# Kernel tuning notes

Hardware: AMD Instinct MI355X
Metric: run time of the kernel (lower is better)

The kernel has to match this reference:

```python
import jax, jax.numpy as jnp
import numpy as np

B, S, T = 64, 128, 64
V, E, H, L = 32000, 512, 512, 2
PAD, BOS = 0, 1


def setup_inputs() -> dict:
    key = jax.random.key(0)
    ks = jax.random.split(key, 14)
    w = lambda k, shape: (jax.random.normal(k, shape, jnp.float32) * 0.05)
    src_emb = w(ks[0], (V, E)).at[PAD].set(0.0)
    tgt_emb = w(ks[1], (V, E)).at[PAD].set(0.0)
    enc_Wih = w(ks[2], (L, 4 * H, E))
    enc_Whh = w(ks[3], (L, 4 * H, H))
    enc_b = w(ks[4], (L, 4 * H))          # b_ih + b_hh fused
    dec_Wih = w(ks[5], (L, 4 * H, E))
    dec_Whh = w(ks[6], (L, 4 * H, H))
    dec_b = w(ks[7], (L, 4 * H))
    gen_W = w(ks[8], (V, H))
    gen_b = jnp.zeros((V,), jnp.float32)
    x_seqs = jax.random.randint(ks[9], (B, S), 0, V, jnp.int32)
    x_len = jnp.sort(jax.random.randint(ks[10], (B,), 1, S + 1, jnp.int32))[::-1]
    y_seqs = jax.random.randint(ks[11], (B, T), 0, V, jnp.int32)
    teacher = jax.random.randint(ks[12], (T - 1,), 0, 2, jnp.int32)
    return dict(x_seqs=x_seqs, x_len=x_len, y_seqs=y_seqs, teacher=teacher,
                src_emb=src_emb, tgt_emb=tgt_emb,
                enc_Wih=enc_Wih, enc_Whh=enc_Whh, enc_b=enc_b,
                dec_Wih=dec_Wih, dec_Whh=dec_Whh, dec_b=dec_b,
                gen_W=gen_W, gen_b=gen_b)


def lstm_cell(x, h, c, Wih, Whh, b):
    # torch gate order: i, f, g, o
    g = x @ Wih.T + h @ Whh.T + b
    i, f, gg, o = jnp.split(g, 4, axis=-1)
    c2 = jax.nn.sigmoid(f) * c + jax.nn.sigmoid(i) * jnp.tanh(gg)
    h2 = jax.nn.sigmoid(o) * jnp.tanh(c2)
    return h2, c2


def encode(x_seqs, x_len, src_emb, Wih, Whh, b):
    emb = src_emb[x_seqs]                                  # [B,S,E]
    mask = jnp.arange(S)[None, :] < x_len[:, None]         # [B,S] valid steps
    inp = emb.transpose(1, 0, 2)                           # [S,B,E]
    m_t = mask.T                                           # [S,B]
    hs, cs = [], []
    for l in range(L):
        def step(carry, xs, l=l):
            h, c = carry
            xt, m = xs
            h2, c2 = lstm_cell(xt, h, c, Wih[l], Whh[l], b[l])
            m = m[:, None]
            h2 = jnp.where(m, h2, h)   # freeze state past sequence length
            c2 = jnp.where(m, c2, c)
            return (h2, c2), h2
        z = jnp.zeros((B, H), inp.dtype)
        (hT, cT), out = jax.lax.scan(step, (z, z), (inp, m_t))
        inp = out
        hs.append(hT)
        cs.append(cT)
    return jnp.stack(hs), jnp.stack(cs)                    # each [L,B,H]


def reference(x_seqs, x_len, y_seqs, teacher, src_emb, tgt_emb,
              enc_Wih, enc_Whh, enc_b, dec_Wih, dec_Whh, dec_b, gen_W, gen_b):
    h0, c0 = encode(x_seqs, x_len, src_emb, enc_Wih, enc_Whh, enc_b)

    def step(carry, xs):
        h, c, inp = carry                                  # [L,B,H],[L,B,H],[B]
        y_t, tf = xs                                       # [B], scalar flag
        x = tgt_emb[inp]                                   # [B,E]
        new_h, new_c = [], []
        for l in range(L):
            hl, cl = lstm_cell(x, h[l], c[l], dec_Wih[l], dec_Whh[l], dec_b[l])
            new_h.append(hl); new_c.append(cl)
            x = hl
        logp = jax.nn.log_softmax(x @ gen_W.T + gen_b, axis=-1)   # [B,V]
        expct = jnp.take_along_axis(logp, y_t[:, None], axis=1)[:, 0]
        pred = jnp.argmax(logp, axis=1).astype(inp.dtype)
        nxt = jnp.where(tf > 0, y_t, pred)                 # scheduled sampling
        return (jnp.stack(new_h), jnp.stack(new_c), nxt), expct

    inp0 = jnp.full((B,), BOS, jnp.int32)
    _, outp = jax.lax.scan(step, (h0, c0, inp0), (y_seqs[:, 1:].T, teacher))
    return outp.T                                          # [B, T-1]
```

## Files before the change

kernel.cpp:

```cpp
#include <hip/hip_runtime.h>
#include <hip/hip_bf16.h>
#include <cstdint>
#include <cstddef>

namespace {

constexpr int B = 64, S = 128, T = 64, V = 32000, E = 512, H = 512;
constexpr int G4 = 2048;
constexpr int TM1 = T - 1;
constexpr int CHUNK = 32;
constexpr int BH = B * H;
constexpr int NT = 128;
constexpr int NTILES = V / NT;
constexpr float MARGIN = 0.02f;

typedef __attribute__((ext_vector_type(8))) short short8v;
typedef __attribute__((ext_vector_type(4))) float f32x4;

struct Partial { float top1, top2; int i1, i2; float sumexp, gold; };

__device__ __forceinline__ float sigf(float x) { return 1.0f / (1.0f + expf(-x)); }

__device__ __forceinline__ void split3(float w, __hip_bfloat16& a, __hip_bfloat16& b,
                                       __hip_bfloat16& c2) {
    a = __float2bfloat16(w);
    float r = w - __bfloat162float(a);
    b = __float2bfloat16(r);
    c2 = __float2bfloat16(r - __bfloat162float(b));
}

__global__ __launch_bounds__(256)
void split_dec_k(const float* __restrict__ Wih, const float* __restrict__ Whh,
                 const float* __restrict__ bsrc,
                 __hip_bfloat16* __restrict__ P0, __hip_bfloat16* __restrict__ P1,
                 __hip_bfloat16* __restrict__ P2, float* __restrict__ bint)
{
    int row = blockIdx.x;
    int l = row >> 11, jp = row & 2047;
    int kh = jp >> 2, g = jp & 3, src = g * 512 + kh;
    const float* wih = Wih + ((size_t)l * 2048 + src) * 512;
    const float* whh = Whh + ((size_t)l * 2048 + src) * 512;
    size_t ro = (size_t)row * 1024;
    for (int k = threadIdx.x; k < 1024; k += 256) {
        float w = (k < 512) ? whh[k] : wih[k - 512];
        __hip_bfloat16 a, b, c2; split3(w, a, b, c2);
        P0[ro + k] = a; P1[ro + k] = b; P2[ro + k] = c2;
    }
    if (threadIdx.x == 0) bint[row] = bsrc[l * 2048 + src];
}

__global__ __launch_bounds__(256)
void split_enc_k(const float* __restrict__ Whh,
                 __hip_bfloat16* __restrict__ P0, __hip_bfloat16* __restrict__ P1,
                 __hip_bfloat16* __restrict__ P2)
{
    int row = blockIdx.x;
    int l = row >> 11, jp = row & 2047;
    int kh = jp >> 2, g = jp & 3, src = g * 512 + kh;
    const float* whh = Whh + ((size_t)l * 2048 + src) * 512;
    size_t ro = (size_t)row * 512;
    for (int k = threadIdx.x; k < 512; k += 256) {
        __hip_bfloat16 a, b, c2; split3(whh[k], a, b, c2);
        P0[ro + k] = a; P1[ro + k] = b; P2[ro + k] = c2;
    }
}

__global__ __launch_bounds__(256)
void gemm_k(const float* __restrict__ A, const float* __restrict__ Wt,
            const float* __restrict__ bias, float* __restrict__ C,
            int N, int tokmode, const int* __restrict__ xseq, int m0)
{
    constexpr int K = 512, BM = 64, BN = 128, BK = 16;
    __shared__ __align__(16) float As[BK][BM + 4];
    __shared__ __align__(16) float Bs[BK][BN + 4];
    int tid = threadIdx.x;
    int bm = blockIdx.y * BM, bn = blockIdx.x * BN;
    int tx = tid & 15, ty = tid >> 4;
    float acc[4][8] = {};

    int lm = tid >> 2, lk = (tid & 3) << 2;
    const float* Arow;
    {
        int m = bm + lm;
        if (tokmode) { int mg = m0 + m; int tt = mg >> 6, b = mg & 63;
                       Arow = A + (size_t)xseq[b * S + tt] * K; }
        else Arow = A + (size_t)m * K;
    }
    int ln = tid >> 1, lkb = (tid & 1) << 3;
    const float* Brow = Wt + (size_t)(bn + ln) * K;

    for (int k0 = 0; k0 < K; k0 += BK) {
        float4 av = *(const float4*)(Arow + k0 + lk);
        As[lk + 0][lm] = av.x; As[lk + 1][lm] = av.y;
        As[lk + 2][lm] = av.z; As[lk + 3][lm] = av.w;
        float4 bv0 = *(const float4*)(Brow + k0 + lkb);
        float4 bv1 = *(const float4*)(Brow + k0 + lkb + 4);
        Bs[lkb + 0][ln] = bv0.x; Bs[lkb + 1][ln] = bv0.y;
        Bs[lkb + 2][ln] = bv0.z; Bs[lkb + 3][ln] = bv0.w;
        Bs[lkb + 4][ln] = bv1.x; Bs[lkb + 5][ln] = bv1.y;
        Bs[lkb + 6][ln] = bv1.z; Bs[lkb + 7][ln] = bv1.w;
        __syncthreads();
#pragma unroll
        for (int kk = 0; kk < BK; ++kk) {
            const float4 a4  = *(const float4*)&As[kk][ty * 4];
            const float4 b4a = *(const float4*)&Bs[kk][tx * 8];
            const float4 b4b = *(const float4*)&Bs[kk][tx * 8 + 4];
            const float a[4]  = {a4.x, a4.y, a4.z, a4.w};
            const float bb[8] = {b4a.x, b4a.y, b4a.z, b4a.w,
                                 b4b.x, b4b.y, b4b.z, b4b.w};
#pragma unroll
            for (int i = 0; i < 4; ++i)
#pragma unroll
                for (int j = 0; j < 8; ++j)
                    acc[i][j] = fmaf(a[i], bb[j], acc[i][j]);
        }
        __syncthreads();
    }
#pragma unroll
    for (int i = 0; i < 4; ++i) {
        size_t crow = (size_t)(bm + ty * 4 + i) * N;
#pragma unroll
        for (int j = 0; j < 8; ++j) {
            int cg = bn + tx * 8 + j;
            int jp = ((cg & 511) << 2) | (cg >> 9);
            C[crow + jp] = acc[i][j] + bias[cg];
        }
    }
}

template<int KHALF, bool ENC>
__global__ __launch_bounds__(256)
void step_k(const __hip_bfloat16* __restrict__ hA0, const __hip_bfloat16* __restrict__ hA1,
            const __hip_bfloat16* __restrict__ hA2,
            const __hip_bfloat16* __restrict__ xA0, const __hip_bfloat16* __restrict__ xA1,
            const __hip_bfloat16* __restrict__ xA2,
            const __hip_bfloat16* __restrict__ W0, const __hip_bfloat16* __restrict__ W1,
            const __hip_bfloat16* __restrict__ W2,
            const float* __restrict__ XcOrBias,
            const float* __restrict__ h_in, float* __restrict__ h_out,
            float* __restrict__ c,
            __hip_bfloat16* __restrict__ o0, __hip_bfloat16* __restrict__ o1,
            __hip_bfloat16* __restrict__ o2,
            float* __restrict__ out0, const int* __restrict__ x_len, int t, int tloc)
{
    __shared__ float gs[64][17];
    int tid = threadIdx.x;
    int wave = tid >> 6, lane = tid & 63;
    int lr = lane & 15, kg = (lane >> 4) * 8;
    int arow = wave * 16 + lr;
    int brow = blockIdx.x * 16 + lr;
    const int KW = 512 * KHALF;

    f32x4 acc0 = {0,0,0,0}, acc1 = {0,0,0,0}, acc2 = {0,0,0,0};
    const size_t aoff = (size_t)arow * 512 + kg;
    const size_t boff = (size_t)brow * KW + kg;

#pragma unroll
    for (int kk = 0; kk < KHALF * 16; ++kk) {
        int k0 = kk * 32;
        const __hip_bfloat16 *A0, *A1, *A2; int ka;
        if (KHALF == 2 && kk >= 16) { A0 = xA0; A1 = xA1; A2 = xA2; ka = k0 - 512; }
        else                        { A0 = hA0; A1 = hA1; A2 = hA2; ka = k0; }
        short8v a0 = *(const short8v*)(A0 + aoff + ka);
        short8v a1 = *(const short8v*)(A1 + aoff + ka);
        short8v a2 = *(const short8v*)(A2 + aoff + ka);
        short8v b0 = *(const short8v*)(W0 + boff + k0);
        short8v b1 = *(const short8v*)(W1 + boff + k0);
        short8v b2 = *(const short8v*)(W2 + boff + k0);
        acc0 = __builtin_amdgcn_mfma_f32_16x16x32_bf16(a0, b0, acc0, 0, 0, 0);
        acc1 = __builtin_amdgcn_mfma_f32_16x16x32_bf16(a0, b1, acc1, 0, 0, 0);
        acc2 = __builtin_amdgcn_mfma_f32_16x16x32_bf16(a1, b0, acc2, 0, 0, 0);
        acc0 = __builtin_amdgcn_mfma_f32_16x16x32_bf16(a1, b1, acc0, 0, 0, 0);
        acc1 = __builtin_amdgcn_mfma_f32_16x16x32_bf16(a0, b2, acc1, 0, 0, 0);
        acc2 = __builtin_amdgcn_mfma_f32_16x16x32_bf16(a2, b0, acc2, 0, 0, 0);
    }
    int rb = (lane >> 4) * 4;
#pragma unroll
    for (int r = 0; r < 4; ++r)
        gs[wave * 16 + rb + r][lr] = acc0[r] + acc1[r] + acc2[r];
    __syncthreads();

    int b = tid >> 2, khl = tid & 3;
    int khg = blockIdx.x * 4 + khl;
    float4 add;
    if (ENC) add = *(const float4*)(XcOrBias + (size_t)b * G4 + (size_t)khg * 4);
    else     add = *(const float4*)(XcOrBias + (size_t)khg * 4);
    float gi = gs[b][khl * 4 + 0] + add.x;
    float gf = gs[b][khl * 4 + 1] + add.y;
    float gg = gs[b][khl * 4 + 2] + add.z;
    float go = gs[b][khl * 4 + 3] + add.w;
    size_t idx = (size_t)b * H + khg;
    float cold = c[idx];
    float c2 = sigf(gf) * cold + sigf(gi) * tanhf(gg);
    float h2 = sigf(go) * tanhf(c2);
    if (ENC) {
        bool mk = t < x_len[b];
        if (!mk) { h2 = h_in[idx]; c2 = cold; }
    }
    h_out[idx] = h2;
    c[idx] = c2;
    __hip_bfloat16 s0, s1, s2; split3(h2, s0, s1, s2);
    o0[idx] = s0; o1[idx] = s1; o2[idx] = s2;
    if (ENC && out0) out0[(size_t)(t * B + b) * H + khg] = h2;
}

__global__ __launch_bounds__(256)
void convert_bf16_k(const float* __restrict__ src, __hip_bfloat16* __restrict__ dst, int n)
{
    int i = (blockIdx.x * 256 + threadIdx.x) * 8;
    if (i + 8 > n) return;
    float4 a = *(const float4*)(src + i);
    float4 b = *(const float4*)(src + i + 4);
    __hip_bfloat16 tmp[8];
    tmp[0] = __float2bfloat16(a.x); tmp[1] = __float2bfloat16(a.y);
    tmp[2] = __float2bfloat16(a.z); tmp[3] = __float2bfloat16(a.w);
    tmp[4] = __float2bfloat16(b.x); tmp[5] = __float2bfloat16(b.y);
    tmp[6] = __float2bfloat16(b.z); tmp[7] = __float2bfloat16(b.w);
    *(short8v*)(dst + i) = *(const short8v*)tmp;
}

__global__ __launch_bounds__(256)
void gen_fused_k(const __hip_bfloat16* __restrict__ hbf,
                 const __hip_bfloat16* __restrict__ Wbf,
                 const float* __restrict__ genb,
                 const int* __restrict__ y_seqs, int t,
                 Partial* __restrict__ part)
{
    __shared__ float lds[64][NT + 4];
    __shared__ float pv1[64][4], pv2[64][4], psum[64][4], mrow[64];
    __shared__ int   pi1[64][4], pi2[64][4];

    int tid = threadIdx.x;
    int wave = tid >> 6, lane = tid & 63;
    int n0 = blockIdx.x * NT;
    int lr = lane & 15;
    int kg = (lane >> 4) * 8;

    f32x4 acc[4][2];
    const f32x4 zero = {0.f, 0.f, 0.f, 0.f};
#pragma unroll
    for (int i = 0; i < 4; ++i)
#pragma unroll
        for (int j = 0; j < 2; ++j) acc[i][j] = zero;

    const __hip_bfloat16* Arow = hbf + (size_t)lr * 512 + kg;
    const __hip_bfloat16* Brow = Wbf + (size_t)(n0 + wave * 32 + lr) * 512 + kg;
    for (int k0 = 0; k0 < 512; k0 += 32) {
        short8v a[4], b[2];
#pragma unroll
        for (int mf = 0; mf < 4; ++mf)
            a[mf] = *(const short8v*)(Arow + (size_t)mf * 16 * 512 + k0);
#pragma unroll
        for (int nf = 0; nf < 2; ++nf)
            b[nf] = *(const short8v*)(Brow + (size_t)nf * 16 * 512 + k0);
#pragma unroll
        for (int mf = 0; mf < 4; ++mf)
#pragma unroll
            for (int nf = 0; nf < 2; ++nf)
                acc[mf][nf] = __builtin_amdgcn_mfma_f32_16x16x32_bf16(
                    a[mf], b[nf], acc[mf][nf], 0, 0, 0);
    }
#pragma unroll
    for (int nf = 0; nf < 2; ++nf) {
        int colLocal = wave * 32 + nf * 16 + lr;
        float bias = genb[n0 + colLocal];
#pragma unroll
        for (int mf = 0; mf < 4; ++mf) {
#pragma unroll
            for (int r = 0; r < 4; ++r) {
                int row = mf * 16 + (lane >> 4) * 4 + r;
                lds[row][colLocal] = acc[mf][nf][r] + bias;
            }
        }
    }
    __syncthreads();

    int row = tid >> 2, q = tid & 3;
    int cbase = q * 32;
    float v1 = -3.4e38f, v2 = -3.4e38f; int i1 = 0x7fffffff, i2 = 0x7fffffff;
    for (int c = 0; c < 32; ++c) {
        float v = lds[row][cbase + c];
        int ci = cbase + c;
        if (v > v1 || (v == v1 && ci < i1)) { v2 = v1; i2 = i1; v1 = v; i1 = ci; }
        else if (v > v2 || (v == v2 && ci < i2)) { v2 = v; i2 = ci; }
    }
    pv1[row][q] = v1; pi1[row][q] = i1; pv2[row][q] = v2; pi2[row][q] = i2;
    __syncthreads();

    float t1 = -3.4e38f, t2 = -3.4e38f; int j1 = 0x7fffffff, j2 = 0x7fffffff;
    if (q == 0) {
        for (int k = 0; k < 4; ++k) {
            float a1 = pv1[row][k]; int a1i = pi1[row][k];
            float a2 = pv2[row][k]; int a2i = pi2[row][k];
            if (a1 > t1 || (a1 == t1 && a1i < j1)) { t2 = t1; j2 = j1; t1 = a1; j1 = a1i; }
            else if (a1 > t2 || (a1 == t2 && a1i < j2)) { t2 = a1; j2 = a1i; }
            if (a2 > t1 || (a2 == t1 && a2i < j1)) { t2 = t1; j2 = j1; t1 = a2; j1 = a2i; }
            else if (a2 > t2 || (a2 == t2 && a2i < j2)) { t2 = a2; j2 = a2i; }
        }
        mrow[row] = t1;
    }
    __syncthreads();
    float m = mrow[row];
    float s = 0.f;
    for (int c = 0; c < 32; ++c) s += expf(lds[row][cbase + c] - m);
    psum[row][q] = s;
    __syncthreads();
    if (q == 0) {
        float sum = psum[row][0] + psum[row][1] + psum[row][2] + psum[row][3];
        Partial p;
        p.top1 = t1; p.top2 = t2; p.i1 = n0 + j1; p.i2 = n0 + j2;
        p.sumexp = sum; p.gold = 0.f;
        part[(size_t)blockIdx.x * B + row] = p;
    }
}

__global__ __launch_bounds__(256)
void dec_reduce2_k(const Partial* __restrict__ part,
                   const float* __restrict__ h,
                   const float* __restrict__ genW, const float* __restrict__ genb,
                   const float* __restrict__ tgt_emb,
                   const int* __restrict__ y_seqs, const int* __restrict__ teacher,
                   float* __restrict__ outp,
                   __hip_bfloat16* __restrict__ xp0, __hip_bfloat16* __restrict__ xp1,
                   __hip_bfloat16* __restrict__ xp2, int t)
{
    __shared__ float sM[256], sS[256], red[256];
    __shared__ float cV[16], rV[16];
    __shared__ int   cI[16];
    __shared__ int   cN, nxt;
    int b = blockIdx.x, tid = threadIdx.x;
    int y = y_seqs[b * T + t + 1];
    const float* hrow = h + (size_t)b * 512;

    float M = -3.4e38f;
    for (int i = tid; i < NTILES; i += 256) M = fmaxf(M, part[(size_t)i * B + b].top1);
    sM[tid] = M; __syncthreads();
    for (int o = 128; o; o >>= 1) { if (tid < o) sM[tid] = fmaxf(sM[tid], sM[tid + o]); __syncthreads(); }
    M = sM[0];
    if (tid == 0) cN = 0;
    __syncthreads();

    float Ssum = 0.f;
    for (int i = tid; i < NTILES; i += 256) {
        Partial p = part[(size_t)i * B + b];
        Ssum += p.sumexp * expf(p.top1 - M);
        if (p.top1 >= M - MARGIN) { int j = atomicAdd(&cN, 1); if (j < 16) { cV[j] = p.top1; cI[j] = p.i1; } }
        if (p.top2 >= M - MARGIN) { int j = atomicAdd(&cN, 1); if (j < 16) { cV[j] = p.top2; cI[j] = p.i2; } }
    }
    sS[tid] = Ssum; __syncthreads();
    for (int o = 128; o; o >>= 1) { if (tid < o) sS[tid] += sS[tid + o]; __syncthreads(); }
    float lse = M + logf(sS[0]);
    int nc = cN < 16 ? cN : 16;

    {
        const float* wrow = genW + (size_t)y * 512;
        float s = 0.f;
        for (int k = tid; k < 512; k += 256) s = fmaf(hrow[k], wrow[k], s);
        red[tid] = s; __syncthreads();
        for (int o = 128; o; o >>= 1) { if (tid < o) red[tid] += red[tid + o]; __syncthreads(); }
        if (tid == 0) outp[b * TM1 + t] = red[0] + genb[y] - lse;
        __syncthreads();
    }
    if (nc > 1) {
        for (int j = 0; j < nc; ++j) {
            const float* wrow = genW + (size_t)cI[j] * 512;
            float s = 0.f;
            for (int k = tid; k < 512; k += 256) s = fmaf(hrow[k], wrow[k], s);
            red[tid] = s; __syncthreads();
            for (int o = 128; o; o >>= 1) { if (tid < o) red[tid] += red[tid + o]; __syncthreads(); }
            if (tid == 0) rV[j] = red[0] + genb[cI[j]];
            __syncthreads();
        }
    }
    if (tid == 0) {
        int winner;
        if (nc == 1) winner = cI[0];
        else {
            float bv = -3.4e38f; int bi = 0x7fffffff;
            for (int j = 0; j < nc; ++j)
                if (rV[j] > bv || (rV[j] == bv && cI[j] < bi)) { bv = rV[j]; bi = cI[j]; }
            winner = bi;
        }
        nxt = (teacher[t] > 0) ? y : winner;
    }
    __syncthreads();
    int tok = nxt;
    for (int k = tid; k < 512; k += 256) {
        float w = tgt_emb[(size_t)tok * 512 + k];
        __hip_bfloat16 s0, s1, s2; split3(w, s0, s1, s2);
        xp0[(size_t)b * 512 + k] = s0;
        xp1[(size_t)b * 512 + k] = s1;
        xp2[(size_t)b * 512 + k] = s2;
    }
}

__global__ __launch_bounds__(256)
void init_x_k(const float* __restrict__ tgt_emb,
              __hip_bfloat16* __restrict__ xp0, __hip_bfloat16* __restrict__ xp1,
              __hip_bfloat16* __restrict__ xp2)
{
    int b = blockIdx.x;
    for (int k = threadIdx.x; k < 512; k += 256) {
        float w = tgt_emb[512 + k];
        __hip_bfloat16 s0, s1, s2; split3(w, s0, s1, s2);
        xp0[(size_t)b * 512 + k] = s0;
        xp1[(size_t)b * 512 + k] = s1;
        xp2[(size_t)b * 512 + k] = s2;
    }
}

}

extern "C" void kernel_launch(void* const* d_in, const int* in_sizes, int n_in,
                              void* d_out, int out_size, void* d_ws, size_t ws_size,
                              hipStream_t stream)
{
    (void)in_sizes; (void)n_in; (void)out_size;
    const int*   x_seqs  = (const int*)  d_in[0];
    const int*   x_len   = (const int*)  d_in[1];
    const int*   y_seqs  = (const int*)  d_in[2];
    const int*   teacher = (const int*)  d_in[3];
    const float* src_emb = (const float*)d_in[4];
    const float* tgt_emb = (const float*)d_in[5];
    const float* eWih    = (const float*)d_in[6];
    const float* eWhh    = (const float*)d_in[7];
    const float* eb      = (const float*)d_in[8];
    const float* dWih    = (const float*)d_in[9];
    const float* dWhh    = (const float*)d_in[10];
    const float* db      = (const float*)d_in[11];
    const float* genW    = (const float*)d_in[12];
    const float* genb    = (const float*)d_in[13];
    float* out = (float*)d_out;

    float* w = (float*)d_ws;
    size_t off = 0;
    auto take = [&](size_t n) { float* p = w + off; off += n; return p; };
    auto takeb = [&](size_t n) { return (__hip_bfloat16*)take((n + 1) / 2); };

    float* Xc     = take((size_t)CHUNK * B * G4);
    float* out0   = take((size_t)S * B * H);
    __hip_bfloat16* eP0 = takeb((size_t)2 * G4 * 512);
    __hip_bfloat16* eP1 = takeb((size_t)2 * G4 * 512);
    __hip_bfloat16* eP2 = takeb((size_t)2 * G4 * 512);
    __hip_bfloat16* dP0 = takeb((size_t)2 * G4 * 1024);
    __hip_bfloat16* dP1 = takeb((size_t)2 * G4 * 1024);
    __hip_bfloat16* dP2 = takeb((size_t)2 * G4 * 1024);
    float* bint   = take(2 * (size_t)G4);
    float* hping  = take(2 * (size_t)BH);
    float* cenc   = take(2 * (size_t)BH);
    float* decc   = take(2 * (size_t)BH);
    float* dech0  = take((size_t)BH);
    float* dech1  = take((size_t)BH);
    __hip_bfloat16* encP   = takeb((size_t)2 * 3 * BH);
    __hip_bfloat16* decL0P = takeb((size_t)2 * 3 * BH);
    __hip_bfloat16* decL1P = takeb((size_t)2 * 3 * BH);
    __hip_bfloat16* xP     = takeb((size_t)3 * BH);
    float* part_f = take((size_t)NTILES * B * 6);
    if (ws_size < off * sizeof(float)) return;

    __hip_bfloat16* Wbf = (__hip_bfloat16*)Xc;
    Partial* part = (Partial*)part_f;
    auto encPl = [&](int slot, int pl) { return encP   + ((size_t)slot * 3 + pl) * BH; };
    auto d0Pl  = [&](int slot, int pl) { return decL0P + ((size_t)slot * 3 + pl) * BH; };
    auto d1Pl  = [&](int slot, int pl) { return decL1P + ((size_t)slot * 3 + pl) * BH; };

    dim3 tpb256(256);

    split_enc_k<<<dim3(2 * G4), tpb256, 0, stream>>>(eWhh, eP0, eP1, eP2);
    split_dec_k<<<dim3(2 * G4), tpb256, 0, stream>>>(dWih, dWhh, db, dP0, dP1, dP2, bint);
    hipMemsetAsync(hping, 0, 2 * BH * sizeof(float), stream);
    hipMemsetAsync(cenc,  0, 2 * BH * sizeof(float), stream);

    for (int l = 0; l < 2; ++l) {
        const float* WihL = eWih + (size_t)l * G4 * E;
        const float* bL   = eb + l * G4;
        const __hip_bfloat16* W0 = eP0 + (size_t)l * G4 * 512;
        const __hip_bfloat16* W1 = eP1 + (size_t)l * G4 * 512;
        const __hip_bfloat16* W2 = eP2 + (size_t)l * G4 * 512;
        float* cL = cenc + (size_t)l * BH;
        float* o0 = (l == 0) ? out0 : nullptr;
        hipMemsetAsync(encP, 0, 3 * BH * sizeof(__hip_bfloat16), stream);
        for (int c0 = 0; c0 < S; c0 += CHUNK) {
            if (l == 0)
                gemm_k<<<dim3(G4 / 128, CHUNK * B / 64), tpb256, 0, stream>>>(
                    src_emb, WihL, bL, Xc, G4, 1, x_seqs, c0 * B);
            else
                gemm_k<<<dim3(G4 / 128, CHUNK * B / 64), tpb256, 0, stream>>>(
                    out0 + (size_t)c0 * B * H, WihL, bL, Xc, G4, 0, nullptr, 0);
            for (int t = c0; t < c0 + CHUNK; ++t) {
                int si = t & 1, so = (t + 1) & 1;
                step_k<1, true><<<dim3(128), tpb256, 0, stream>>>(
                    encPl(si, 0), encPl(si, 1), encPl(si, 2),
                    nullptr, nullptr, nullptr, W0, W1, W2,
                    Xc + (size_t)(t - c0) * B * G4,
                    hping + (size_t)si * BH, hping + (size_t)so * BH, cL,
                    encPl(so, 0), encPl(so, 1), encPl(so, 2),
                    o0, x_len, t, t - c0);
            }
        }
        hipMemcpyAsync((l == 0 ? decL0P : decL1P), encP,
                       3 * BH * sizeof(__hip_bfloat16), hipMemcpyDeviceToDevice, stream);
        hipMemcpyAsync(decc + (size_t)l * BH, cL, BH * sizeof(float),
                       hipMemcpyDeviceToDevice, stream);
        if (l == 0) hipMemsetAsync(hping, 0, 2 * BH * sizeof(float), stream);
    }

    convert_bf16_k<<<dim3(V * E / 2048), tpb256, 0, stream>>>(genW, Wbf, V * E);
    init_x_k<<<dim3(B), tpb256, 0, stream>>>(tgt_emb, xP, xP + BH, xP + 2 * BH);

    for (int t = 0; t < TM1; ++t) {
        int si = t & 1, so = (t + 1) & 1;
        step_k<2, false><<<dim3(128), tpb256, 0, stream>>>(
            d0Pl(si, 0), d0Pl(si, 1), d0Pl(si, 2),
            xP, xP + BH, xP + 2 * BH,
            dP0, dP1, dP2, bint,
            nullptr, dech0, decc,
            d0Pl(so, 0), d0Pl(so, 1), d0Pl(so, 2),
            nullptr, nullptr, 0, 0);
        step_k<2, false><<<dim3(128), tpb256, 0, stream>>>(
            d1Pl(si, 0), d1Pl(si, 1), d1Pl(si, 2),
            d0Pl(so, 0), d0Pl(so, 1), d0Pl(so, 2),
            dP0 + (size_t)G4 * 1024, dP1 + (size_t)G4 * 1024, dP2 + (size_t)G4 * 1024,
            bint + G4,
            nullptr, dech1, decc + BH,
            d1Pl(so, 0), d1Pl(so, 1), d1Pl(so, 2),
            nullptr, nullptr, 0, 0);
        gen_fused_k<<<dim3(NTILES), tpb256, 0, stream>>>(
            d1Pl(so, 0), Wbf, genb, y_seqs, t, part);
        dec_reduce2_k<<<dim3(B), tpb256, 0, stream>>>(
            part, dech1, genW, genb, tgt_emb, y_seqs, teacher, out,
            xP, xP + BH, xP + 2 * BH, t);
    }
}
```

Before: 10.46 ms.

## Fuse all encoder/decoder steps into one persistent kernel with grid barriers

Replaces the hundreds of per-timestep kernel launches (encoder GEMMs and steps, decoder steps, generator tiles, reductions) with one persistent kernel of 256 blocks. Stages are separated by a software grid barrier built on agent-scope atomics, and shared memory is drawn from a pool of per-stage structs. The goal is to remove launch overhead and inter-kernel gaps on the long sequential recurrence. In exchange, idle blocks wait at every barrier. The kernel also depends on all 256 blocks being co-resident, or it can deadlock. The generator stage now runs 250 tiles on 256 blocks.

```diff
diff --git a/kernel.cpp b/kernel.cpp
--- a/kernel.cpp
+++ b/kernel.cpp
@@ -13,11 +13,20 @@
 constexpr int NT = 128;
 constexpr int NTILES = V / NT;
 constexpr float MARGIN = 0.02f;
+constexpr unsigned NBLK = 256;
 
 typedef __attribute__((ext_vector_type(8))) short short8v;
 typedef __attribute__((ext_vector_type(4))) float f32x4;
 
 struct Partial { float top1, top2; int i1, i2; float sumexp, gold; };
+
+struct GemmSh { float As[16][68]; float Bs[16][132]; };
+struct StepSh { float gs[64][17]; };
+struct GenSh  { float lds[64][NT + 4]; float pv1[64][4], pv2[64][4], psum[64][4], mrow[64];
+                int pi1[64][4], pi2[64][4]; };
+struct RedSh  { float sM[256], sS[256], red[256]; float cV[16], rV[16]; int cI[16]; int cN, nxt; };
+static_assert(sizeof(GenSh) < 40960 && sizeof(GemmSh) < 40960 &&
+              sizeof(StepSh) < 40960 && sizeof(RedSh) < 40960, "shared pool");
 
 __device__ __forceinline__ float sigf(float x) { return 1.0f / (1.0f + expf(-x)); }
 
@@ -27,6 +36,24 @@
     float r = w - __bfloat162float(a);
     b = __float2bfloat16(r);
     c2 = __float2bfloat16(r - __bfloat162float(b));
+}
+
+__device__ __forceinline__ void gbar(unsigned* cnt, unsigned* gen, unsigned& ep)
+{
+    unsigned tgt = ep + 1; ep = tgt;
+    __syncthreads();
+    if (threadIdx.x == 0) {
+        unsigned prev = __hip_atomic_fetch_add(cnt, 1u, __ATOMIC_ACQ_REL, __HIP_MEMORY_SCOPE_AGENT);
+        if (prev == NBLK - 1u) {
+            __hip_atomic_store(cnt, 0u, __ATOMIC_RELAXED, __HIP_MEMORY_SCOPE_AGENT);
+            __hip_atomic_store(gen, tgt, __ATOMIC_RELEASE, __HIP_MEMORY_SCOPE_AGENT);
+        } else {
+            while (__hip_atomic_load(gen, __ATOMIC_RELAXED, __HIP_MEMORY_SCOPE_AGENT) < tgt)
+                __builtin_amdgcn_s_sleep(2);
+            __builtin_amdgcn_fence(__ATOMIC_ACQUIRE, "agent");
+        }
+    }
+    __syncthreads();
 }
 
 __global__ __launch_bounds__(256)
@@ -65,16 +92,15 @@
     }
 }
 
-__global__ __launch_bounds__(256)
-void gemm_k(const float* __restrict__ A, const float* __restrict__ Wt,
-            const float* __restrict__ bias, float* __restrict__ C,
-            int N, int tokmode, const int* __restrict__ xseq, int m0)
-{
-    constexpr int K = 512, BM = 64, BN = 128, BK = 16;
-    __shared__ __align__(16) float As[BK][BM + 4];
-    __shared__ __align__(16) float Bs[BK][BN + 4];
+__device__ void gemm_tile(char* shraw, const float* __restrict__ A,
+                          const float* __restrict__ Wt, const float* __restrict__ bias,
+                          float* __restrict__ C, int tokmode,
+                          const int* __restrict__ xseq, int m0, int bx, int by)
+{
+    GemmSh* sh = reinterpret_cast<GemmSh*>(shraw);
+    constexpr int K = 512, BK = 16;
     int tid = threadIdx.x;
-    int bm = blockIdx.y * BM, bn = blockIdx.x * BN;
+    int bm = by * 64, bn = bx * 128;
     int tx = tid & 15, ty = tid >> 4;
     float acc[4][8] = {};
 
@@ -91,20 +117,20 @@
 
     for (int k0 = 0; k0 < K; k0 += BK) {
         float4 av = *(const float4*)(Arow + k0 + lk);
-        As[lk + 0][lm] = av.x; As[lk + 1][lm] = av.y;
-        As[lk + 2][lm] = av.z; As[lk + 3][lm] = av.w;
+        sh->As[lk + 0][lm] = av.x; sh->As[lk + 1][lm] = av.y;
+        sh->As[lk + 2][lm] = av.z; sh->As[lk + 3][lm] = av.w;
         float4 bv0 = *(const float4*)(Brow + k0 + lkb);
         float4 bv1 = *(const float4*)(Brow + k0 + lkb + 4);
-        Bs[lkb + 0][ln] = bv0.x; Bs[lkb + 1][ln] = bv0.y;
-        Bs[lkb + 2][ln] = bv0.z; Bs[lkb + 3][ln] = bv0.w;
-        Bs[lkb + 4][ln] = bv1.x; Bs[lkb + 5][ln] = bv1.y;
-        Bs[lkb + 6][ln] = bv1.z; Bs[lkb + 7][ln] = bv1.w;
+        sh->Bs[lkb + 0][ln] = bv0.x; sh->Bs[lkb + 1][ln] = bv0.y;
+        sh->Bs[lkb + 2][ln] = bv0.z; sh->Bs[lkb + 3][ln] = bv0.w;
+        sh->Bs[lkb + 4][ln] = bv1.x; sh->Bs[lkb + 5][ln] = bv1.y;
+        sh->Bs[lkb + 6][ln] = bv1.z; sh->Bs[lkb + 7][ln] = bv1.w;
         __syncthreads();
 #pragma unroll
         for (int kk = 0; kk < BK; ++kk) {
-            const float4 a4  = *(const float4*)&As[kk][ty * 4];
-            const float4 b4a = *(const float4*)&Bs[kk][tx * 8];
-            const float4 b4b = *(const float4*)&Bs[kk][tx * 8 + 4];
+            const float4 a4  = *(const float4*)&sh->As[kk][ty * 4];
+            const float4 b4a = *(const float4*)&sh->Bs[kk][tx * 8];
+            const float4 b4b = *(const float4*)&sh->Bs[kk][tx * 8 + 4];
             const float a[4]  = {a4.x, a4.y, a4.z, a4.w};
             const float bb[8] = {b4a.x, b4a.y, b4a.z, b4a.w,
                                  b4b.x, b4b.y, b4b.z, b4b.w};
@@ -118,7 +144,7 @@
     }
 #pragma unroll
     for (int i = 0; i < 4; ++i) {
-        size_t crow = (size_t)(bm + ty * 4 + i) * N;
+        size_t crow = (size_t)(bm + ty * 4 + i) * G4;
 #pragma unroll
         for (int j = 0; j < 8; ++j) {
             int cg = bn + tx * 8 + j;
@@ -129,26 +155,25 @@
 }
 
 template<int KHALF, bool ENC>
-__global__ __launch_bounds__(256)
-void step_k(const __hip_bfloat16* __restrict__ hA0, const __hip_bfloat16* __restrict__ hA1,
-            const __hip_bfloat16* __restrict__ hA2,
-            const __hip_bfloat16* __restrict__ xA0, const __hip_bfloat16* __restrict__ xA1,
-            const __hip_bfloat16* __restrict__ xA2,
-            const __hip_bfloat16* __restrict__ W0, const __hip_bfloat16* __restrict__ W1,
-            const __hip_bfloat16* __restrict__ W2,
-            const float* __restrict__ XcOrBias,
-            const float* __restrict__ h_in, float* __restrict__ h_out,
-            float* __restrict__ c,
-            __hip_bfloat16* __restrict__ o0, __hip_bfloat16* __restrict__ o1,
-            __hip_bfloat16* __restrict__ o2,
-            float* __restrict__ out0, const int* __restrict__ x_len, int t, int tloc)
-{
-    __shared__ float gs[64][17];
+__device__ void step_body(char* shraw, int blk,
+    const __hip_bfloat16* __restrict__ hA0, const __hip_bfloat16* __restrict__ hA1,
+    const __hip_bfloat16* __restrict__ hA2,
+    const __hip_bfloat16* __restrict__ xA0, const __hip_bfloat16* __restrict__ xA1,
+    const __hip_bfloat16* __restrict__ xA2,
+    const __hip_bfloat16* __restrict__ W0, const __hip_bfloat16* __restrict__ W1,
+    const __hip_bfloat16* __restrict__ W2,
+    const float* __restrict__ XcOrBias, const float* __restrict__ h_in,
+    float* __restrict__ h_out, float* __restrict__ c,
+    __hip_bfloat16* __restrict__ o0, __hip_bfloat16* __restrict__ o1,
+    __hip_bfloat16* __restrict__ o2,
+    float* __restrict__ out0, const int* __restrict__ x_len, int t)
+{
+    StepSh* sh = reinterpret_cast<StepSh*>(shraw);
     int tid = threadIdx.x;
     int wave = tid >> 6, lane = tid & 63;
     int lr = lane & 15, kg = (lane >> 4) * 8;
     int arow = wave * 16 + lr;
-    int brow = blockIdx.x * 16 + lr;
+    int brow = blk * 16 + lr;
     const int KW = 512 * KHALF;
 
     f32x4 acc0 = {0,0,0,0}, acc1 = {0,0,0,0}, acc2 = {0,0,0,0};
@@ -177,18 +202,18 @@
     int rb = (lane >> 4) * 4;
 #pragma unroll
     for (int r = 0; r < 4; ++r)
-        gs[wave * 16 + rb + r][lr] = acc0[r] + acc1[r] + acc2[r];
+        sh->gs[wave * 16 + rb + r][lr] = acc0[r] + acc1[r] + acc2[r];
     __syncthreads();
 
     int b = tid >> 2, khl = tid & 3;
-    int khg = blockIdx.x * 4 + khl;
+    int khg = blk * 4 + khl;
     float4 add;
     if (ENC) add = *(const float4*)(XcOrBias + (size_t)b * G4 + (size_t)khg * 4);
     else     add = *(const float4*)(XcOrBias + (size_t)khg * 4);
-    float gi = gs[b][khl * 4 + 0] + add.x;
-    float gf = gs[b][khl * 4 + 1] + add.y;
-    float gg = gs[b][khl * 4 + 2] + add.z;
-    float go = gs[b][khl * 4 + 3] + add.w;
+    float gi = sh->gs[b][khl * 4 + 0] + add.x;
+    float gf = sh->gs[b][khl * 4 + 1] + add.y;
+    float gg = sh->gs[b][khl * 4 + 2] + add.z;
+    float go = sh->gs[b][khl * 4 + 3] + add.w;
     size_t idx = (size_t)b * H + khg;
     float cold = c[idx];
     float c2 = sigf(gf) * cold + sigf(gi) * tanhf(gg);
@@ -204,35 +229,16 @@
     if (ENC && out0) out0[(size_t)(t * B + b) * H + khg] = h2;
 }
 
-__global__ __launch_bounds__(256)
-void convert_bf16_k(const float* __restrict__ src, __hip_bfloat16* __restrict__ dst, int n)
-{
-    int i = (blockIdx.x * 256 + threadIdx.x) * 8;
-    if (i + 8 > n) return;
-    float4 a = *(const float4*)(src + i);
-    float4 b = *(const float4*)(src + i + 4);
-    __hip_bfloat16 tmp[8];
-    tmp[0] = __float2bfloat16(a.x); tmp[1] = __float2bfloat16(a.y);
-    tmp[2] = __float2bfloat16(a.z); tmp[3] = __float2bfloat16(a.w);
-    tmp[4] = __float2bfloat16(b.x); tmp[5] = __float2bfloat16(b.y);
-    tmp[6] = __float2bfloat16(b.z); tmp[7] = __float2bfloat16(b.w);
-    *(short8v*)(dst + i) = *(const short8v*)tmp;
-}
-
-__global__ __launch_bounds__(256)
-void gen_fused_k(const __hip_bfloat16* __restrict__ hbf,
-                 const __hip_bfloat16* __restrict__ Wbf,
-                 const float* __restrict__ genb,
-                 const int* __restrict__ y_seqs, int t,
-                 Partial* __restrict__ part)
-{
-    __shared__ float lds[64][NT + 4];
-    __shared__ float pv1[64][4], pv2[64][4], psum[64][4], mrow[64];
-    __shared__ int   pi1[64][4], pi2[64][4];
-
+__device__ void gen_body(char* shraw, int bid,
+                         const __hip_bfloat16* __restrict__ hbf,
+                         const __hip_bfloat16* __restrict__ Wbf,
+                         const float* __restrict__ genb,
+                         Partial* __restrict__ part)
+{
+    GenSh* sh = reinterpret_cast<GenSh*>(shraw);
     int tid = threadIdx.x;
     int wave = tid >> 6, lane = tid & 63;
-    int n0 = blockIdx.x * NT;
+    int n0 = bid * NT;
     int lr = lane & 15;
     int kg = (lane >> 4) * 8;
 
@@ -269,7 +275,7 @@
 #pragma unroll
             for (int r = 0; r < 4; ++r) {
                 int row = mf * 16 + (lane >> 4) * 4 + r;
-                lds[row][colLocal] = acc[mf][nf][r] + bias;
+                sh->lds[row][colLocal] = acc[mf][nf][r] + bias;
             }
         }
     }
@@ -279,112 +285,109 @@
     int cbase = q * 32;
     float v1 = -3.4e38f, v2 = -3.4e38f; int i1 = 0x7fffffff, i2 = 0x7fffffff;
     for (int c = 0; c < 32; ++c) {
-        float v = lds[row][cbase + c];
+        float v = sh->lds[row][cbase + c];
         int ci = cbase + c;
         if (v > v1 || (v == v1 && ci < i1)) { v2 = v1; i2 = i1; v1 = v; i1 = ci; }
         else if (v > v2 || (v == v2 && ci < i2)) { v2 = v; i2 = ci; }
     }
-    pv1[row][q] = v1; pi1[row][q] = i1; pv2[row][q] = v2; pi2[row][q] = i2;
+    sh->pv1[row][q] = v1; sh->pi1[row][q] = i1; sh->pv2[row][q] = v2; sh->pi2[row][q] = i2;
     __syncthreads();
 
     float t1 = -3.4e38f, t2 = -3.4e38f; int j1 = 0x7fffffff, j2 = 0x7fffffff;
     if (q == 0) {
         for (int k = 0; k < 4; ++k) {
-            float a1 = pv1[row][k]; int a1i = pi1[row][k];
-            float a2 = pv2[row][k]; int a2i = pi2[row][k];
+            float a1 = sh->pv1[row][k]; int a1i = sh->pi1[row][k];
+            float a2 = sh->pv2[row][k]; int a2i = sh->pi2[row][k];
             if (a1 > t1 || (a1 == t1 && a1i < j1)) { t2 = t1; j2 = j1; t1 = a1; j1 = a1i; }
             else if (a1 > t2 || (a1 == t2 && a1i < j2)) { t2 = a1; j2 = a1i; }
             if (a2 > t1 || (a2 == t1 && a2i < j1)) { t2 = t1; j2 = j1; t1 = a2; j1 = a2i; }
             else if (a2 > t2 || (a2 == t2 && a2i < j2)) { t2 = a2; j2 = a2i; }
         }
-        mrow[row] = t1;
-    }
-    __syncthreads();
-    float m = mrow[row];
+        sh->mrow[row] = t1;
+    }
+    __syncthreads();
+    float m = sh->mrow[row];
     float s = 0.f;
-    for (int c = 0; c < 32; ++c) s += expf(lds[row][cbase + c] - m);
-    psum[row][q] = s;
+    for (int c = 0; c < 32; ++c) s += expf(sh->lds[row][cbase + c] - m);
+    sh->psum[row][q] = s;
     __syncthreads();
     if (q == 0) {
-        float sum = psum[row][0] + psum[row][1] + psum[row][2] + psum[row][3];
+        float sum = sh->psum[row][0] + sh->psum[row][1] + sh->psum[row][2] + sh->psum[row][3];
         Partial p;
         p.top1 = t1; p.top2 = t2; p.i1 = n0 + j1; p.i2 = n0 + j2;
         p.sumexp = sum; p.gold = 0.f;
-        part[(size_t)blockIdx.x * B + row] = p;
-    }
-}
-
-__global__ __launch_bounds__(256)
-void dec_reduce2_k(const Partial* __restrict__ part,
-                   const float* __restrict__ h,
-                   const float* __restrict__ genW, const float* __restrict__ genb,
-                   const float* __restrict__ tgt_emb,
-                   const int* __restrict__ y_seqs, const int* __restrict__ teacher,
-                   float* __restrict__ outp,
-                   __hip_bfloat16* __restrict__ xp0, __hip_bfloat16* __restrict__ xp1,
-                   __hip_bfloat16* __restrict__ xp2, int t)
-{
-    __shared__ float sM[256], sS[256], red[256];
-    __shared__ float cV[16], rV[16];
-    __shared__ int   cI[16];
-    __shared__ int   cN, nxt;
-    int b = blockIdx.x, tid = threadIdx.x;
+        part[(size_t)bid * B + row] = p;
+    }
+}
+
+__device__ void reduce_body(char* shraw, int b,
+                            const Partial* __restrict__ part,
+                            const float* __restrict__ h,
+                            const float* __restrict__ genW, const float* __restrict__ genb,
+                            const float* __restrict__ tgt_emb,
+                            const int* __restrict__ y_seqs, const int* __restrict__ teacher,
+                            float* __restrict__ outp,
+                            __hip_bfloat16* __restrict__ xp0, __hip_bfloat16* __restrict__ xp1,
+                            __hip_bfloat16* __restrict__ xp2, int t)
+{
+    RedSh* sh = reinterpret_cast<RedSh*>(shraw);
+    int tid = threadIdx.x;
     int y = y_seqs[b * T + t + 1];
     const float* hrow = h + (size_t)b * 512;
 
     float M = -3.4e38f;
     for (int i = tid; i < NTILES; i += 256) M = fmaxf(M, part[(size_t)i * B + b].top1);
-    sM[tid] = M; __syncthreads();
-    for (int o = 128; o; o >>= 1) { if (tid < o) sM[tid] = fmaxf(sM[tid], sM[tid + o]); __syncthreads(); }
-    M = sM[0];
-    if (tid == 0) cN = 0;
+    sh->sM[tid] = M; __syncthreads();
+    for (int o = 128; o; o >>= 1) { if (tid < o) sh->sM[tid] = fmaxf(sh->sM[tid], sh->sM[tid + o]); __syncthreads(); }
+    M = sh->sM[0];
+    if (tid == 0) sh->cN = 0;
     __syncthreads();
 
     float Ssum = 0.f;
     for (int i = tid; i < NTILES; i += 256) {
         Partial p = part[(size_t)i * B + b];
         Ssum += p.sumexp * expf(p.top1 - M);
-        if (p.top1 >= M - MARGIN) { int j = atomicAdd(&cN, 1); if (j < 16) { cV[j] = p.top1; cI[j] = p.i1; } }
-        if (p.top2 >= M - MARGIN) { int j = atomicAdd(&cN, 1); if (j < 16) { cV[j] = p.top2; cI[j] = p.i2; } }
-    }
-    sS[tid] = Ssum; __syncthreads();
-    for (int o = 128; o; o >>= 1) { if (tid < o) sS[tid] += sS[tid + o]; __syncthreads(); }
-    float lse = M + logf(sS[0]);
-    int nc = cN < 16 ? cN : 16;
+        if (p.top1 >= M - MARGIN) { int j = atomicAdd(&sh->cN, 1); if (j < 16) { sh->cV[j] = p.top1; sh->cI[j] = p.i1; } }
+        if (p.top2 >= M - MARGIN) { int j = atomicAdd(&sh->cN, 1); if (j < 16) { sh->cV[j] = p.top2; sh->cI[j] = p.i2; } }
+    }
+    sh->sS[tid] = Ssum; __syncthreads();
+    for (int o = 128; o; o >>= 1) { if (tid < o) sh->sS[tid] += sh->sS[tid + o]; __syncthreads(); }
+    float lse = M + logf(sh->sS[0]);
+    int nc = sh->cN < 16 ? sh->cN : 16;
 
     {
         const float* wrow = genW + (size_t)y * 512;
         float s = 0.f;
         for (int k = tid; k < 512; k += 256) s = fmaf(hrow[k], wrow[k], s);
-        red[tid] = s; __syncthreads();
-        for (int o = 128; o; o >>= 1) { if (tid < o) red[tid] += red[tid + o]; __syncthreads(); }
-        if (tid == 0) outp[b * TM1 + t] = red[0] + genb[y] - lse;
+        sh->red[tid] = s; __syncthreads();
+        for (int o = 128; o; o >>= 1) { if (tid < o) sh->red[tid] += sh->red[tid + o]; __syncthreads(); }
+        if (tid == 0) outp[b * TM1 + t] = sh->red[0] + genb[y] - lse;
         __syncthreads();
     }
     if (nc > 1) {
         for (int j = 0; j < nc; ++j) {
-            const float* wrow = genW + (size_t)cI[j] * 512;
+            const float* wrow = genW + (size_t)sh->cI[j] * 512;
             float s = 0.f;
             for (int k = tid; k < 512; k += 256) s = fmaf(hrow[k], wrow[k], s);
-            red[tid] = s; __syncthreads();
-            for (int o = 128; o; o >>= 1) { if (tid < o) red[tid] += red[tid + o]; __syncthreads(); }
-            if (tid == 0) rV[j] = red[0] + genb[cI[j]];
+            sh->red[tid] = s; __syncthreads();
+            for (int o = 128; o; o >>= 1) { if (tid < o) sh->red[tid] += sh->red[tid + o]; __syncthreads(); }
+            if (tid == 0) sh->rV[j] = sh->red[0] + genb[sh->cI[j]];
             __syncthreads();
         }
     }
     if (tid == 0) {
         int winner;
-        if (nc == 1) winner = cI[0];
+        if (nc == 1) winner = sh->cI[0];
         else {
             float bv = -3.4e38f; int bi = 0x7fffffff;
             for (int j = 0; j < nc; ++j)
-                if (rV[j] > bv || (rV[j] == bv && cI[j] < bi)) { bv = rV[j]; bi = cI[j]; }
+                if (sh->rV[j] > bv || (sh->rV[j] == bv && sh->cI[j] < bi)) { bv = sh->rV[j]; bi = sh->cI[j]; }
             winner = bi;
         }
-        nxt = (teacher[t] > 0) ? y : winner;
-    }
-    __syncthreads();
-    int tok = nxt;
+        sh->nxt = (teacher[t] > 0) ? y : winner;
+    }
+    __syncthreads();
+    int tok = sh->nxt;
     for (int k = tid; k < 512; k += 256) {
         float w = tgt_emb[(size_t)tok * 512 + k];
         __hip_bfloat16 s0, s1, s2; split3(w, s0, s1, s2);
@@ -394,18 +397,130 @@
     }
 }
 
-__global__ __launch_bounds__(256)
-void init_x_k(const float* __restrict__ tgt_emb,
-              __hip_bfloat16* __restrict__ xp0, __hip_bfloat16* __restrict__ xp1,
-              __hip_bfloat16* __restrict__ xp2)
-{
-    int b = blockIdx.x;
-    for (int k = threadIdx.x; k < 512; k += 256) {
-        float w = tgt_emb[512 + k];
-        __hip_bfloat16 s0, s1, s2; split3(w, s0, s1, s2);
-        xp0[(size_t)b * 512 + k] = s0;
-        xp1[(size_t)b * 512 + k] = s1;
-        xp2[(size_t)b * 512 + k] = s2;
+struct Args {
+    const int *x_seqs, *x_len, *y_seqs, *teacher;
+    const float *src_emb, *tgt_emb, *eWih, *eb, *genW, *genb;
+    float *Xc, *out0;
+    const __hip_bfloat16 *eP0, *eP1, *eP2, *dP0, *dP1, *dP2;
+    const float* bint;
+    float *hping, *cenc, *decc, *dech0, *dech1;
+    __hip_bfloat16 *encP, *decL0P, *decL1P, *xP, *Wbf;
+    Partial* part;
+    float* outp;
+    unsigned *cnt, *gen;
+};
+
+__global__ __launch_bounds__(256, 1)
+void persist_k(Args a)
+{
+    __shared__ __align__(16) char shpool[40960];
+    unsigned ep = 0;
+    const int bid = blockIdx.x;
+    const int tid = threadIdx.x;
+    const int gtid = bid * 256 + tid;
+    const int GS = NBLK * 256;
+
+    auto encPl = [&](int slot, int pl) { return a.encP   + ((size_t)slot * 3 + pl) * BH; };
+    auto d0Pl  = [&](int slot, int pl) { return a.decL0P + ((size_t)slot * 3 + pl) * BH; };
+    auto d1Pl  = [&](int slot, int pl) { return a.decL1P + ((size_t)slot * 3 + pl) * BH; };
+
+    for (int i = gtid; i < 2 * BH; i += GS) { a.hping[i] = 0.f; a.cenc[i] = 0.f; }
+    for (int i = gtid; i < 3 * BH / 2; i += GS) ((uint32_t*)a.encP)[i] = 0u;
+    gbar(a.cnt, a.gen, ep);
+
+    for (int l = 0; l < 2; ++l) {
+        const float* WihL = a.eWih + (size_t)l * G4 * E;
+        const float* bL   = a.eb + l * G4;
+        const __hip_bfloat16* W0 = a.eP0 + (size_t)l * G4 * 512;
+        const __hip_bfloat16* W1 = a.eP1 + (size_t)l * G4 * 512;
+        const __hip_bfloat16* W2 = a.eP2 + (size_t)l * G4 * 512;
+        float* cL = a.cenc + (size_t)l * BH;
+        float* o0 = (l == 0) ? a.out0 : nullptr;
+        for (int c0 = 0; c0 < S; c0 += CHUNK) {
+            for (int tile = bid; tile < 512; tile += NBLK) {
+                int by = tile >> 4, bx = tile & 15;
+                gemm_tile(shpool, (l == 0) ? a.src_emb : a.out0 + (size_t)c0 * B * H,
+                          WihL, bL, a.Xc, l == 0, a.x_seqs, c0 * B, bx, by);
+            }
+            gbar(a.cnt, a.gen, ep);
+            for (int t = c0; t < c0 + CHUNK; ++t) {
+                int si = t & 1, so = si ^ 1;
+                if (bid < 128)
+                    step_body<1, true>(shpool, bid,
+                        encPl(si, 0), encPl(si, 1), encPl(si, 2),
+                        nullptr, nullptr, nullptr, W0, W1, W2,
+                        a.Xc + (size_t)(t - c0) * B * G4,
+                        a.hping + (size_t)si * BH, a.hping + (size_t)so * BH, cL,
+                        encPl(so, 0), encPl(so, 1), encPl(so, 2),
+                        o0, a.x_len, t);
+                gbar(a.cnt, a.gen, ep);
+            }
+        }
+        {
+            __hip_bfloat16* dst = (l == 0) ? a.decL0P : a.decL1P;
+            const uint32_t* s32 = (const uint32_t*)a.encP;
+            uint32_t* d32 = (uint32_t*)dst;
+            for (int i = gtid; i < 3 * BH / 2; i += GS) d32[i] = s32[i];
+            for (int i = gtid; i < BH; i += GS) a.decc[(size_t)l * BH + i] = cL[i];
+        }
+        gbar(a.cnt, a.gen, ep);
+        if (l == 0) {
+            for (int i = gtid; i < 2 * BH; i += GS) a.hping[i] = 0.f;
+            for (int i = gtid; i < 3 * BH / 2; i += GS) ((uint32_t*)a.encP)[i] = 0u;
+        }
+        gbar(a.cnt, a.gen, ep);
+    }
+
+    {
+        const int N8 = V * E / 8;
+        for (int i = gtid; i < N8; i += GS) {
+            float4 x = *(const float4*)(a.genW + (size_t)i * 8);
+            float4 y = *(const float4*)(a.genW + (size_t)i * 8 + 4);
+            __hip_bfloat16 tmp[8];
+            tmp[0] = __float2bfloat16(x.x); tmp[1] = __float2bfloat16(x.y);
+            tmp[2] = __float2bfloat16(x.z); tmp[3] = __float2bfloat16(x.w);
+            tmp[4] = __float2bfloat16(y.x); tmp[5] = __float2bfloat16(y.y);
+            tmp[6] = __float2bfloat16(y.z); tmp[7] = __float2bfloat16(y.w);
+            *(short8v*)(a.Wbf + (size_t)i * 8) = *(const short8v*)tmp;
+        }
+        for (int i = gtid; i < BH; i += GS) {
+            int k = i & 511;
+            float w = a.tgt_emb[512 + k];
+            __hip_bfloat16 s0, s1, s2; split3(w, s0, s1, s2);
+            a.xP[i] = s0; a.xP[BH + i] = s1; a.xP[2 * BH + i] = s2;
+        }
+    }
+    gbar(a.cnt, a.gen, ep);
+
+    for (int t = 0; t < TM1; ++t) {
+        int si = t & 1, so = si ^ 1;
+        if (bid < 128)
+            step_body<2, false>(shpool, bid,
+                d0Pl(si, 0), d0Pl(si, 1), d0Pl(si, 2),
+                a.xP, a.xP + BH, a.xP + 2 * BH,
+                a.dP0, a.dP1, a.dP2, a.bint,
+                nullptr, a.dech0, a.decc,
+                d0Pl(so, 0), d0Pl(so, 1), d0Pl(so, 2),
+                nullptr, nullptr, 0);
+        gbar(a.cnt, a.gen, ep);
+        if (bid < 128)
+            step_body<2, false>(shpool, bid,
+                d1Pl(si, 0), d1Pl(si, 1), d1Pl(si, 2),
+                d0Pl(so, 0), d0Pl(so, 1), d0Pl(so, 2),
+                a.dP0 + (size_t)G4 * 1024, a.dP1 + (size_t)G4 * 1024,
+                a.dP2 + (size_t)G4 * 1024, a.bint + G4,
+                nullptr, a.dech1, a.decc + BH,
+                d1Pl(so, 0), d1Pl(so, 1), d1Pl(so, 2),
+                nullptr, nullptr, 0);
+        gbar(a.cnt, a.gen, ep);
+        if (bid < NTILES)
+            gen_body(shpool, bid, d1Pl(so, 0), a.Wbf, a.genb, a.part);
+        gbar(a.cnt, a.gen, ep);
+        if (bid < B)
+            reduce_body(shpool, bid, a.part, a.dech1, a.genW, a.genb, a.tgt_emb,
+                        a.y_seqs, a.teacher, a.outp,
+                        a.xP, a.xP + BH, a.xP + 2 * BH, t);
+        gbar(a.cnt, a.gen, ep);
     }
 }
 
@@ -430,13 +545,13 @@
     const float* db      = (const float*)d_in[11];
     const float* genW    = (const float*)d_in[12];
     const float* genb    = (const float*)d_in[13];
-    float* out = (float*)d_out;
 
     float* w = (float*)d_ws;
     size_t off = 0;
     auto take = [&](size_t n) { float* p = w + off; off += n; return p; };
     auto takeb = [&](size_t n) { return (__hip_bfloat16*)take((n + 1) / 2); };
 
+    unsigned* barst = (unsigned*)take(64);
     float* Xc     = take((size_t)CHUNK * B * G4);
     float* out0   = take((size_t)S * B * H);
     __hip_bfloat16* eP0 = takeb((size_t)2 * G4 * 512);
@@ -458,77 +573,25 @@
     float* part_f = take((size_t)NTILES * B * 6);
     if (ws_size < off * sizeof(float)) return;
 
-    __hip_bfloat16* Wbf = (__hip_bfloat16*)Xc;
-    Partial* part = (Partial*)part_f;
-    auto encPl = [&](int slot, int pl) { return encP   + ((size_t)slot * 3 + pl) * BH; };
-    auto d0Pl  = [&](int slot, int pl) { return decL0P + ((size_t)slot * 3 + pl) * BH; };
-    auto d1Pl  = [&](int slot, int pl) { return decL1P + ((size_t)slot * 3 + pl) * BH; };
-
     dim3 tpb256(256);
-
     split_enc_k<<<dim3(2 * G4), tpb256, 0, stream>>>(eWhh, eP0, eP1, eP2);
     split_dec_k<<<dim3(2 * G4), tpb256, 0, stream>>>(dWih, dWhh, db, dP0, dP1, dP2, bint);
-    hipMemsetAsync(hping, 0, 2 * BH * sizeof(float), stream);
-    hipMemsetAsync(cenc,  0, 2 * BH * sizeof(float), stream);
-
-    for (int l = 0; l < 2; ++l) {
-        const float* WihL = eWih + (size_t)l * G4 * E;
-        const float* bL   = eb + l * G4;
-        const __hip_bfloat16* W0 = eP0 + (size_t)l * G4 * 512;
-        const __hip_bfloat16* W1 = eP1 + (size_t)l * G4 * 512;
-        const __hip_bfloat16* W2 = eP2 + (size_t)l * G4 * 512;
-        float* cL = cenc + (size_t)l * BH;
-        float* o0 = (l == 0) ? out0 : nullptr;
-        hipMemsetAsync(encP, 0, 3 * BH * sizeof(__hip_bfloat16), stream);
-        for (int c0 = 0; c0 < S; c0 += CHUNK) {
-            if (l == 0)
-                gemm_k<<<dim3(G4 / 128, CHUNK * B / 64), tpb256, 0, stream>>>(
-                    src_emb, WihL, bL, Xc, G4, 1, x_seqs, c0 * B);
-            else
-                gemm_k<<<dim3(G4 / 128, CHUNK * B / 64), tpb256, 0, stream>>>(
-                    out0 + (size_t)c0 * B * H, WihL, bL, Xc, G4, 0, nullptr, 0);
-            for (int t = c0; t < c0 + CHUNK; ++t) {
-                int si = t & 1, so = (t + 1) & 1;
-                step_k<1, true><<<dim3(128), tpb256, 0, stream>>>(
-                    encPl(si, 0), encPl(si, 1), encPl(si, 2),
-                    nullptr, nullptr, nullptr, W0, W1, W2,
-                    Xc + (size_t)(t - c0) * B * G4,
-                    hping + (size_t)si * BH, hping + (size_t)so * BH, cL,
-                    encPl(so, 0), encPl(so, 1), encPl(so, 2),
-                    o0, x_len, t, t - c0);
-            }
-        }
-        hipMemcpyAsync((l == 0 ? decL0P : decL1P), encP,
-                       3 * BH * sizeof(__hip_bfloat16), hipMemcpyDeviceToDevice, stream);
-        hipMemcpyAsync(decc + (size_t)l * BH, cL, BH * sizeof(float),
-                       hipMemcpyDeviceToDevice, stream);
-        if (l == 0) hipMemsetAsync(hping, 0, 2 * BH * sizeof(float), stream);
-    }
-
-    convert_bf16_k<<<dim3(V * E / 2048), tpb256, 0, stream>>>(genW, Wbf, V * E);
-    init_x_k<<<dim3(B), tpb256, 0, stream>>>(tgt_emb, xP, xP + BH, xP + 2 * BH);
-
-    for (int t = 0; t < TM1; ++t) {
-        int si = t & 1, so = (t + 1) & 1;
-        step_k<2, false><<<dim3(128), tpb256, 0, stream>>>(
-            d0Pl(si, 0), d0Pl(si, 1), d0Pl(si, 2),
-            xP, xP + BH, xP + 2 * BH,
-            dP0, dP1, dP2, bint,
-            nullptr, dech0, decc,
-            d0Pl(so, 0), d0Pl(so, 1), d0Pl(so, 2),
-            nullptr, nullptr, 0, 0);
-        step_k<2, false><<<dim3(128), tpb256, 0, stream>>>(
-            d1Pl(si, 0), d1Pl(si, 1), d1Pl(si, 2),
-            d0Pl(so, 0), d0Pl(so, 1), d0Pl(so, 2),
-            dP0 + (size_t)G4 * 1024, dP1 + (size_t)G4 * 1024, dP2 + (size_t)G4 * 1024,
-            bint + G4,
-            nullptr, dech1, decc + BH,
-            d1Pl(so, 0), d1Pl(so, 1), d1Pl(so, 2),
-            nullptr, nullptr, 0, 0);
-        gen_fused_k<<<dim3(NTILES), tpb256, 0, stream>>>(
-            d1Pl(so, 0), Wbf, genb, y_seqs, t, part);
-        dec_reduce2_k<<<dim3(B), tpb256, 0, stream>>>(
-            part, dech1, genW, genb, tgt_emb, y_seqs, teacher, out,
-            xP, xP + BH, xP + 2 * BH, t);
-    }
-}
+    hipMemsetAsync(barst, 0, 256, stream);
+
+    Args a;
+    a.x_seqs = x_seqs; a.x_len = x_len; a.y_seqs = y_seqs; a.teacher = teacher;
+    a.src_emb = src_emb; a.tgt_emb = tgt_emb; a.eWih = eWih; a.eb = eb;
+    a.genW = genW; a.genb = genb;
+    a.Xc = Xc; a.out0 = out0;
+    a.eP0 = eP0; a.eP1 = eP1; a.eP2 = eP2;
+    a.dP0 = dP0; a.dP1 = dP1; a.dP2 = dP2;
+    a.bint = bint;
+    a.hping = hping; a.cenc = cenc; a.decc = decc; a.dech0 = dech0; a.dech1 = dech1;
+    a.encP = encP; a.decL0P = decL0P; a.decL1P = decL1P; a.xP = xP;
+    a.Wbf = (__hip_bfloat16*)Xc;
+    a.part = (Partial*)part_f;
+    a.outp = (float*)d_out;
+    a.cnt = barst; a.gen = barst + 16;
+
+    persist_k<<<dim3(NBLK), tpb256, 0, stream>>>(a);
+}
```

Measured after the change: 18.55 ms. +77.4%, slower.
